# Optimization experiments

Measured on AMD Instinct MI355X. Metric: run time of the kernel, lower is better.

## Reference

```python
import jax, jax.numpy as jnp
import numpy as np

B, S, E = 4, 2048, 1024
H = 16
D = E // H  # head dim = 64
ROPE_BASE = 10000.0


def _rope(t):
    # t: [B, H, S, D]; rotate-half RoPE (YaRN with scale=1 reduces to this)
    half = D // 2
    inv_freq = 1.0 / (ROPE_BASE ** (jnp.arange(0, half, dtype=jnp.float32) / half))
    pos = jnp.arange(t.shape[2], dtype=jnp.float32)
    ang = pos[:, None] * inv_freq[None, :]          # [S, D/2]
    cos, sin = jnp.cos(ang), jnp.sin(ang)
    t1, t2 = t[..., :half], t[..., half:]
    return jnp.concatenate([t1 * cos - t2 * sin, t1 * sin + t2 * cos], axis=-1)


def setup_inputs() -> dict:
    key = jax.random.key(0)
    ks = jax.random.split(key, 6)
    sc = 1.0 / np.sqrt(E)
    return {
        "x": jax.random.normal(ks[0], (B, S, E), jnp.float32),
        "Wq": jax.random.normal(ks[1], (E, E), jnp.float32) * sc,
        "Wk": jax.random.normal(ks[2], (E, E), jnp.float32) * sc,
        "Wv": jax.random.normal(ks[3], (E, E), jnp.float32) * sc,
        "Wp": jax.random.normal(ks[4], (E, E), jnp.float32) * sc,
        "bp": jnp.zeros((E,), jnp.float32),
    }


def reference(x, Wq, Wk, Wv, Wp, bp):
    seq = x.shape[1]
    def heads(W):
        # project then split heads -> [B, H, S, D]
        return (x @ W.T).reshape(B, seq, H, D).transpose(0, 2, 1, 3)
    q = _rope(heads(Wq))
    k = _rope(heads(Wk))
    v = heads(Wv)
    score = jnp.einsum("bhqd,bhkd->bhqk", q, k) * (D ** -0.5)
    mask = jnp.tril(jnp.ones((seq, seq), dtype=bool))
    score = jnp.where(mask[None, None], score, -jnp.inf)
    attn = jax.nn.softmax(score, axis=-1)
    out = jnp.einsum("bhqk,bhkd->bhqd", attn, v)
    out = out.transpose(0, 2, 1, 3).reshape(B, seq, E)
    return out @ Wp.T + bp  # dropout is identity at inference
```

## Files before the change

### kernel.cpp

```cpp
#include <hip/hip_runtime.h>
#include <hip/hip_bf16.h>

typedef __hip_bfloat16 bf16;
typedef __attribute__((ext_vector_type(8))) short bf16x8;
typedef __attribute__((ext_vector_type(4))) short bf16x4;
typedef __attribute__((ext_vector_type(4))) float f32x4;

static constexpr int B_ = 4, S_ = 2048, E_ = 1024, H_ = 16, D_ = 64;
static constexpr int M_ = B_ * S_;
static constexpr int NQKV = 3 * E_;

__device__ __forceinline__ void gload_lds16(const void* g, void* l) {
  __builtin_amdgcn_global_load_lds(
      (const __attribute__((address_space(1))) unsigned int*)g,
      (__attribute__((address_space(3))) unsigned int*)l, 16, 0, 0);
}

__device__ __forceinline__ void cast8(const float* __restrict__ src,
                                      bf16* __restrict__ dst, int t) {
  float4 a = ((const float4*)src)[2 * t];
  float4 b = ((const float4*)src)[2 * t + 1];
  union { bf16x8 v; bf16 e[8]; } u;
  u.e[0] = __float2bfloat16(a.x); u.e[1] = __float2bfloat16(a.y);
  u.e[2] = __float2bfloat16(a.z); u.e[3] = __float2bfloat16(a.w);
  u.e[4] = __float2bfloat16(b.x); u.e[5] = __float2bfloat16(b.y);
  u.e[6] = __float2bfloat16(b.z); u.e[7] = __float2bfloat16(b.w);
  ((bf16x8*)dst)[t] = u.v;
}

__global__ void prep_kernel(const float* __restrict__ x, const float* __restrict__ Wq,
                            const float* __restrict__ Wk, const float* __restrict__ Wv,
                            const float* __restrict__ Wp,
                            bf16* __restrict__ x_bf, bf16* __restrict__ w_bf,
                            float2* __restrict__ qtab, float2* __restrict__ ktab) {
  int bid = blockIdx.x;
  if (bid < 4096) {
    cast8(x, x_bf, bid * 256 + threadIdx.x);
  } else if (bid < 6144) {
    int wi = (bid - 4096) >> 9;
    const float* src = wi == 0 ? Wq : wi == 1 ? Wk : wi == 2 ? Wv : Wp;
    cast8(src, w_bf + (size_t)wi * E_ * E_, ((bid - 4096) & 511) * 256 + threadIdx.x);
  } else {
    int tt = (bid - 6144) * 256 + threadIdx.x;
    int i = tt & 31, s = tt >> 5;
    float inv_freq = powf(10000.0f, -(float)i / 32.0f);
    float ang = (float)s * inv_freq;
    float c = cosf(ang), sn = sinf(ang);
    const float qsc = 0.18033688011112043f;
    qtab[tt] = make_float2(c * qsc, sn * qsc);
    ktab[tt] = make_float2(c, sn);
  }
}

template <int OUTMODE, int BM>
__launch_bounds__(BM * 2)
__global__ void gemm_bt_kernel(const bf16* __restrict__ A, int lda,
                               const bf16* __restrict__ Bw, int ldb,
                               void* __restrict__ Cv, int ldc,
                               const float* __restrict__ bias,
                               int K, int ntiles_n,
                               const float2* __restrict__ qtab,
                               const float2* __restrict__ ktab,
                               bf16* __restrict__ qh,
                               bf16* __restrict__ khsw,
                               bf16* __restrict__ vtsw) {
  constexpr int NTHR = BM * 2;
  __shared__ bf16 Asm[BM * 64];
  __shared__ bf16 Bsm[128 * 64];
  int t = threadIdx.x;
  int lane = t & 63, wid = t >> 6;
  int wm = wid >> 1, wc = wid & 1;
  int l15 = lane & 15, l4 = lane >> 4;

  int cpx = gridDim.x >> 3;
  int swb = (blockIdx.x & 7) * cpx + (blockIdx.x >> 3);
  int n0 = (swb % ntiles_n) * 128;
  int m0 = (swb / ntiles_n) * BM;

  f32x4 acc[4][4];
#pragma unroll
  for (int i = 0; i < 4; i++)
#pragma unroll
    for (int j = 0; j < 4; j++) acc[i][j] = (f32x4){0.f, 0.f, 0.f, 0.f};

  for (int k0 = 0; k0 < K; k0 += 64) {
#pragma unroll
    for (int p = 0; p < 4; p++) {
      int c = p * NTHR + t;
      int row = c >> 3, kg = c & 7;
      int kgs = kg ^ (row & 7);
      gload_lds16(A + (size_t)(m0 + row) * lda + k0 + kgs * 8, &Asm[c * 8]);
    }
#pragma unroll
    for (int p = 0; p < 1024 / NTHR; p++) {
      int c = p * NTHR + t;
      int row = c >> 3, kg = c & 7;
      int kgs = kg ^ (row & 7);
      gload_lds16(Bw + (size_t)(n0 + row) * ldb + k0 + kgs * 8, &Bsm[c * 8]);
    }
    __syncthreads();
#pragma unroll
    for (int kk = 0; kk < 2; kk++) {
      bf16x8 am[4], bn[4];
#pragma unroll
      for (int i = 0; i < 4; i++) {
        int ra = wm * 64 + i * 16 + l15;
        am[i] = *(const bf16x8*)&Asm[ra * 64 + ((kk * 32 + l4 * 8) ^ ((ra & 7) * 8))];
        int rb = wc * 64 + i * 16 + l15;
        bn[i] = *(const bf16x8*)&Bsm[rb * 64 + ((kk * 32 + l4 * 8) ^ ((rb & 7) * 8))];
      }
#pragma unroll
      for (int i = 0; i < 4; i++)
#pragma unroll
        for (int j = 0; j < 4; j++)
          acc[i][j] = __builtin_amdgcn_mfma_f32_16x16x32_bf16(am[i], bn[j], acc[i][j], 0, 0, 0);
    }
    __syncthreads();
  }

  if (OUTMODE == 1) {
#pragma unroll
    for (int i = 0; i < 4; i++)
#pragma unroll
      for (int j = 0; j < 4; j++)
#pragma unroll
        for (int r = 0; r < 4; r++) {
          int m = m0 + wm * 64 + i * 16 + l4 * 4 + r;
          int n = n0 + wc * 64 + j * 16 + l15;
          ((float*)Cv)[(size_t)m * ldc + n] = acc[i][j][r] + bias[n];
        }
  } else {
    int btype = n0 >> 10;
    int h = ((n0 & 1023) >> 6) + wc;
    if (btype < 2) {
      const float2* tab = (btype == 0) ? qtab : ktab;
#pragma unroll
      for (int i = 0; i < 4; i++) {
        int mbase = m0 + wm * 64 + i * 16 + l4 * 4;
#pragma unroll
        for (int r = 0; r < 4; r++) {
          int m = mbase + r;
          int s = m & 2047, b = m >> 11;
#pragma unroll
          for (int j = 0; j < 2; j++) {
            int d1 = j * 16 + l15;
            float2 cs = tab[s * 32 + d1];
            float t1 = acc[i][j][r], t2 = acc[i][j + 2][r];
            bf16 o1 = __float2bfloat16(t1 * cs.x - t2 * cs.y);
            bf16 o2 = __float2bfloat16(t1 * cs.y + t2 * cs.x);
            if (btype == 0) {
              bf16* dst = qh + ((size_t)(b * H_ + h) * S_ + s) * D_;
              dst[d1] = o1;
              dst[d1 + 32] = o2;
            } else {
              int row = s & 63, kt = s >> 6, sz = (row & 7) * 8;
              bf16* dst = khsw + (((size_t)(b * H_ + h) * 32 + kt) * 64 + row) * 64;
              dst[d1 ^ sz] = o1;
              dst[(d1 + 32) ^ sz] = o2;
            }
          }
        }
      }
    } else {
#pragma unroll
      for (int i = 0; i < 4; i++) {
        int mbase = m0 + wm * 64 + i * 16 + l4 * 4;
        int c0 = mbase & 63, kt = (mbase >> 6) & 31, b = mbase >> 11;
#pragma unroll
        for (int j = 0; j < 4; j++) {
          int d = j * 16 + l15;
          union { bf16x4 v; short e[4]; } pk;
#pragma unroll
          for (int r = 0; r < 4; r++) {
            bf16 tv = __float2bfloat16(acc[i][j][r]);
            pk.e[r] = *(short*)&tv;
          }
          *(bf16x4*)&vtsw[(((size_t)(b * H_ + h) * 32 + kt) * 64 + d) * 64 +
                          (c0 ^ ((d & 7) * 8))] = pk.v;
        }
      }
    }
  }
}

__launch_bounds__(256, 3)
__global__ void attn_kernel(const bf16* __restrict__ qh, const bf16* __restrict__ khsw,
                            const bf16* __restrict__ vtsw, bf16* __restrict__ attn) {
  __shared__ bf16 Ksm[2][4096];
  __shared__ bf16 Vsm[2][4096];
  __shared__ bf16 Plds[4][2][16][64];
  int t = threadIdx.x, lane = t & 63, w = t >> 6;
  int l15 = lane & 15, l4 = lane >> 4;
  int swz = (l15 & 7) * 8;
  int st = 15 - (blockIdx.x >> 6);
  int bh = blockIdx.x & 63;
  int b = bh >> 4, h = bh & 15;
  const bf16* Qh = qh + (size_t)bh * S_ * D_;

#define STAGE(bb, kt)                                                          \
  do {                                                                         \
    const bf16* kb_ = khsw + ((size_t)bh * 32 + (kt)) * 4096 + w * 1024 + lane * 8; \
    const bf16* vb_ = vtsw + ((size_t)bh * 32 + (kt)) * 4096 + w * 1024 + lane * 8; \
    gload_lds16(kb_, &Ksm[bb][w * 1024]);                                      \
    gload_lds16(kb_ + 512, &Ksm[bb][w * 1024 + 512]);                          \
    gload_lds16(vb_, &Vsm[bb][w * 1024]);                                      \
    gload_lds16(vb_ + 512, &Vsm[bb][w * 1024 + 512]);                          \
  } while (0)

  int q0 = st * 128 + w * 32;
  int nt = 2 * st + 2;

  bf16x8 qf[2][2];
#pragma unroll
  for (int qg = 0; qg < 2; qg++)
#pragma unroll
    for (int sl = 0; sl < 2; sl++)
      qf[qg][sl] = *(const bf16x8*)&Qh[(size_t)(q0 + qg * 16 + l15) * D_ + sl * 32 + l4 * 8];

  f32x4 acc_o[2][4];
  float lsum[2] = {0.f, 0.f};
#pragma unroll
  for (int qg = 0; qg < 2; qg++)
#pragma unroll
    for (int j = 0; j < 4; j++) acc_o[qg][j] = (f32x4){0.f, 0.f, 0.f, 0.f};

  STAGE(0, 0);
  __syncthreads();
  int buf = 0;
  for (int ti = 0; ti < nt; ti++) {
    int kb = ti * 64;
    if (ti + 1 < nt) STAGE(buf ^ 1, ti + 1);
    if (kb <= q0 + 31) {
      bool maskt = (kb + 63 > q0);
      f32x4 s[2][4];
      __builtin_amdgcn_s_setprio(1);
#pragma unroll
      for (int cb = 0; cb < 4; cb++) {
        bf16x8 kf0 = *(const bf16x8*)&Ksm[buf][(cb * 16 + l15) * 64 + ((l4 * 8) ^ swz)];
        bf16x8 kf1 = *(const bf16x8*)&Ksm[buf][(cb * 16 + l15) * 64 + ((32 + l4 * 8) ^ swz)];
#pragma unroll
        for (int qg = 0; qg < 2; qg++) {
          f32x4 z = (f32x4){0.f, 0.f, 0.f, 0.f};
          z = __builtin_amdgcn_mfma_f32_16x16x32_bf16(kf0, qf[qg][0], z, 0, 0, 0);
          z = __builtin_amdgcn_mfma_f32_16x16x32_bf16(kf1, qf[qg][1], z, 0, 0, 0);
          s[qg][cb] = z;
        }
      }
      __builtin_amdgcn_s_setprio(0);
#pragma unroll
      for (int qg = 0; qg < 2; qg++) {
        int q = q0 + qg * 16 + l15;
#pragma unroll
        for (int cb = 0; cb < 4; cb++) {
          union { bf16x4 v; short e[4]; } pk;
#pragma unroll
          for (int r = 0; r < 4; r++) {
            float p = exp2f(s[qg][cb][r]);
            if (maskt && (kb + cb * 16 + l4 * 4 + r > q)) p = 0.f;
            lsum[qg] += p;
            bf16 pb16 = __float2bfloat16(p);
            pk.e[r] = *(short*)&pb16;
          }
          *(bf16x4*)&Plds[w][qg][l15][(cb * 16 + l4 * 4) ^ swz] = pk.v;
        }
      }
      __builtin_amdgcn_s_setprio(1);
#pragma unroll
      for (int qg = 0; qg < 2; qg++) {
        bf16x8 pf0 = *(const bf16x8*)&Plds[w][qg][l15][(l4 * 8) ^ swz];
        bf16x8 pf1 = *(const bf16x8*)&Plds[w][qg][l15][(32 + l4 * 8) ^ swz];
#pragma unroll
        for (int db = 0; db < 4; db++) {
          bf16x8 vf0 = *(const bf16x8*)&Vsm[buf][(db * 16 + l15) * 64 + ((l4 * 8) ^ swz)];
          bf16x8 vf1 = *(const bf16x8*)&Vsm[buf][(db * 16 + l15) * 64 + ((32 + l4 * 8) ^ swz)];
          acc_o[qg][db] = __builtin_amdgcn_mfma_f32_16x16x32_bf16(pf0, vf0, acc_o[qg][db], 0, 0, 0);
          acc_o[qg][db] = __builtin_amdgcn_mfma_f32_16x16x32_bf16(pf1, vf1, acc_o[qg][db], 0, 0, 0);
        }
      }
      __builtin_amdgcn_s_setprio(0);
    }
    __syncthreads();
    buf ^= 1;
  }

  float invr[2][4];
#pragma unroll
  for (int qg = 0; qg < 2; qg++) {
    float ls = lsum[qg];
    ls += __shfl_xor(ls, 16, 64);
    ls += __shfl_xor(ls, 32, 64);
    float inv = 1.0f / ls;
#pragma unroll
    for (int r = 0; r < 4; r++) invr[qg][r] = __shfl(inv, l4 * 4 + r, 64);
  }

#pragma unroll
  for (int qg = 0; qg < 2; qg++)
#pragma unroll
    for (int db = 0; db < 4; db++)
#pragma unroll
      for (int r = 0; r < 4; r++) {
        int qa = q0 + qg * 16 + l4 * 4 + r;
        attn[(size_t)(b * S_ + qa) * E_ + h * 64 + db * 16 + l15] =
            __float2bfloat16(acc_o[qg][db][r] * invr[qg][r]);
      }
#undef STAGE
}

extern "C" void kernel_launch(void* const* d_in, const int* in_sizes, int n_in,
                              void* d_out, int out_size, void* d_ws, size_t ws_size,
                              hipStream_t stream) {
  const float* x  = (const float*)d_in[0];
  const float* Wq = (const float*)d_in[1];
  const float* Wk = (const float*)d_in[2];
  const float* Wv = (const float*)d_in[3];
  const float* Wp = (const float*)d_in[4];
  const float* bp = (const float*)d_in[5];

  char* ws = (char*)d_ws;
  bf16* x_bf   = (bf16*)(ws + 0);
  bf16* w_bf   = (bf16*)(ws + (16u << 20));
  bf16* aout   = (bf16*)(ws + (24u << 20));
  bf16* qh     = (bf16*)(ws + (40u << 20));
  bf16* khsw   = (bf16*)(ws + (56u << 20));
  bf16* vtsw   = (bf16*)(ws + (72u << 20));
  float2* qtab = (float2*)(ws + (88u << 20));
  float2* ktab = (float2*)(ws + (88u << 20) + (512u << 10));

  prep_kernel<<<6400, 256, 0, stream>>>(x, Wq, Wk, Wv, Wp, x_bf, w_bf, qtab, ktab);

  gemm_bt_kernel<2, 256><<<(M_ / 256) * (NQKV / 128), 512, 0, stream>>>(
      x_bf, E_, w_bf, E_, nullptr, 0, nullptr, E_, NQKV / 128,
      qtab, ktab, qh, khsw, vtsw);

  attn_kernel<<<16 * 64, 256, 0, stream>>>(qh, khsw, vtsw, aout);

  gemm_bt_kernel<1, 128><<<(M_ / 128) * (E_ / 128), 256, 0, stream>>>(
      aout, E_, w_bf + 3 * (size_t)E_ * E_, E_, d_out, E_, bp, E_, E_ / 128,
      nullptr, nullptr, nullptr, nullptr, nullptr);
}
```

Baseline: 169.8 us.

## Single-buffer V in attention to cut LDS and raise occupancy, reorder block schedule

V tiles are now single-buffered: each V tile is loaded at the start of its own iteration and waited on with an explicit vmcnt plus a barrier before the PV matmul, while K stays double-buffered. This cuts LDS per block so launch bounds can be raised from 3 to 4 blocks per CU. The query-tile order per block index also changes from a plain descending order to a fixed permutation, to balance the causal work across CUs. In exchange, V load latency is only hidden behind the QK and softmax part of the same iteration, and an extra barrier is added per tile.

```diff
diff --git a/kernel.cpp b/kernel.cpp
--- a/kernel.cpp
+++ b/kernel.cpp
@@ -183,28 +183,32 @@
   }
 }
 
-__launch_bounds__(256, 3)
+__launch_bounds__(256, 4)
 __global__ void attn_kernel(const bf16* __restrict__ qh, const bf16* __restrict__ khsw,
                             const bf16* __restrict__ vtsw, bf16* __restrict__ attn) {
   __shared__ bf16 Ksm[2][4096];
-  __shared__ bf16 Vsm[2][4096];
+  __shared__ bf16 Vsm[4096];
   __shared__ bf16 Plds[4][2][16][64];
   int t = threadIdx.x, lane = t & 63, w = t >> 6;
   int l15 = lane & 15, l4 = lane >> 4;
   int swz = (l15 & 7) * 8;
-  int st = 15 - (blockIdx.x >> 6);
+  int g = blockIdx.x >> 6;
+  int st = (int)((0x30214A65B789CDEFull >> (4 * g)) & 15);
   int bh = blockIdx.x & 63;
   int b = bh >> 4, h = bh & 15;
   const bf16* Qh = qh + (size_t)bh * S_ * D_;
 
-#define STAGE(bb, kt)                                                          \
+#define STAGE_K(bb, kt)                                                        \
   do {                                                                         \
     const bf16* kb_ = khsw + ((size_t)bh * 32 + (kt)) * 4096 + w * 1024 + lane * 8; \
-    const bf16* vb_ = vtsw + ((size_t)bh * 32 + (kt)) * 4096 + w * 1024 + lane * 8; \
     gload_lds16(kb_, &Ksm[bb][w * 1024]);                                      \
     gload_lds16(kb_ + 512, &Ksm[bb][w * 1024 + 512]);                          \
-    gload_lds16(vb_, &Vsm[bb][w * 1024]);                                      \
-    gload_lds16(vb_ + 512, &Vsm[bb][w * 1024 + 512]);                          \
+  } while (0)
+#define STAGE_V(kt)                                                            \
+  do {                                                                         \
+    const bf16* vb_ = vtsw + ((size_t)bh * 32 + (kt)) * 4096 + w * 1024 + lane * 8; \
+    gload_lds16(vb_, &Vsm[w * 1024]);                                          \
+    gload_lds16(vb_ + 512, &Vsm[w * 1024 + 512]);                              \
   } while (0)
 
   int q0 = st * 128 + w * 32;
@@ -224,20 +228,23 @@
 #pragma unroll
     for (int j = 0; j < 4; j++) acc_o[qg][j] = (f32x4){0.f, 0.f, 0.f, 0.f};
 
-  STAGE(0, 0);
+  STAGE_K(0, 0);
   __syncthreads();
-  int buf = 0;
+  int kbuf = 0;
   for (int ti = 0; ti < nt; ti++) {
     int kb = ti * 64;
-    if (ti + 1 < nt) STAGE(buf ^ 1, ti + 1);
-    if (kb <= q0 + 31) {
+    bool more = (ti + 1 < nt);
+    STAGE_V(ti);
+    if (more) STAGE_K(kbuf ^ 1, ti + 1);
+    bool act = (kb <= q0 + 31);
+    if (act) {
       bool maskt = (kb + 63 > q0);
       f32x4 s[2][4];
       __builtin_amdgcn_s_setprio(1);
 #pragma unroll
       for (int cb = 0; cb < 4; cb++) {
-        bf16x8 kf0 = *(const bf16x8*)&Ksm[buf][(cb * 16 + l15) * 64 + ((l4 * 8) ^ swz)];
-        bf16x8 kf1 = *(const bf16x8*)&Ksm[buf][(cb * 16 + l15) * 64 + ((32 + l4 * 8) ^ swz)];
+        bf16x8 kf0 = *(const bf16x8*)&Ksm[kbuf][(cb * 16 + l15) * 64 + ((l4 * 8) ^ swz)];
+        bf16x8 kf1 = *(const bf16x8*)&Ksm[kbuf][(cb * 16 + l15) * 64 + ((32 + l4 * 8) ^ swz)];
 #pragma unroll
         for (int qg = 0; qg < 2; qg++) {
           f32x4 z = (f32x4){0.f, 0.f, 0.f, 0.f};
@@ -264,6 +271,15 @@
           *(bf16x4*)&Plds[w][qg][l15][(cb * 16 + l4 * 4) ^ swz] = pk.v;
         }
       }
+    }
+    if (more) {
+      asm volatile("s_waitcnt vmcnt(2)" ::: "memory");
+    } else {
+      asm volatile("s_waitcnt vmcnt(0)" ::: "memory");
+    }
+    __builtin_amdgcn_sched_barrier(0);
+    __builtin_amdgcn_s_barrier();
+    if (act) {
       __builtin_amdgcn_s_setprio(1);
 #pragma unroll
       for (int qg = 0; qg < 2; qg++) {
@@ -271,8 +287,8 @@
         bf16x8 pf1 = *(const bf16x8*)&Plds[w][qg][l15][(32 + l4 * 8) ^ swz];
 #pragma unroll
         for (int db = 0; db < 4; db++) {
-          bf16x8 vf0 = *(const bf16x8*)&Vsm[buf][(db * 16 + l15) * 64 + ((l4 * 8) ^ swz)];
-          bf16x8 vf1 = *(const bf16x8*)&Vsm[buf][(db * 16 + l15) * 64 + ((32 + l4 * 8) ^ swz)];
+          bf16x8 vf0 = *(const bf16x8*)&Vsm[(db * 16 + l15) * 64 + ((l4 * 8) ^ swz)];
+          bf16x8 vf1 = *(const bf16x8*)&Vsm[(db * 16 + l15) * 64 + ((32 + l4 * 8) ^ swz)];
           acc_o[qg][db] = __builtin_amdgcn_mfma_f32_16x16x32_bf16(pf0, vf0, acc_o[qg][db], 0, 0, 0);
           acc_o[qg][db] = __builtin_amdgcn_mfma_f32_16x16x32_bf16(pf1, vf1, acc_o[qg][db], 0, 0, 0);
         }
@@ -280,8 +296,10 @@
       __builtin_amdgcn_s_setprio(0);
     }
     __syncthreads();
-    buf ^= 1;
-  }
+    kbuf ^= 1;
+  }
+#undef STAGE_K
+#undef STAGE_V
 
   float invr[2][4];
 #pragma unroll
@@ -304,7 +322,6 @@
         attn[(size_t)(b * S_ + qa) * E_ + h * 64 + db * 16 + l15] =
             __float2bfloat16(acc_o[qg][db][r] * invr[qg][r]);
       }
-#undef STAGE
 }
 
 extern "C" void kernel_launch(void* const* d_in, const int* in_sizes, int n_in,
```

After: 170.8 us. About the same (+0.6%).
